# Performance work log

Hardware: AMD Instinct MI355X
Metric: run time of the kernel (lower is better)

The kernel has to match this reference:

```python
import jax, jax.numpy as jnp
import numpy as np

MAX_DELAY = 16
BUF_D = MAX_DELAY + 1  # buffer_max_delay
B, S, I, H, C = 32, 256, 128, 512, 64
OUT_LEN = 64


def setup_inputs() -> dict:
    key = jax.random.key(0)
    ks = jax.random.split(key, 12)
    s = 0.02
    return {
        "x": jax.random.normal(ks[0], (B, S, I), jnp.float32),
        "lengths": jax.random.randint(ks[1], (B,), 0, S, jnp.int32),
        "out_lengths": OUT_LEN,
        "W_in": jax.random.normal(ks[2], (I + H, H), jnp.float32) * s,
        "b_in": jnp.zeros((H,), jnp.float32),
        "W_pass": jax.random.normal(ks[3], (H, H), jnp.float32) * s,
        "b_pass": jnp.zeros((H,), jnp.float32),
        "W_tau": jax.random.normal(ks[4], (H, H), jnp.float32) * s,
        "b_tau": jnp.zeros((H,), jnp.float32),
        "W_mem": jax.random.normal(ks[5], (H, H), jnp.float32) * s,
        "b_mem": jnp.zeros((H,), jnp.float32),
        "W_out": jax.random.normal(ks[6], (H, C), jnp.float32) * s,
        "b_out": jnp.zeros((C,), jnp.float32),
    }


def _update_buffer(buffer, hidden, tau, mem_l):
    # buffer: (B,H,BUF_D); hidden,tau,mem_l: (B,H)
    idx = jnp.arange(1, BUF_D, dtype=buffer.dtype)          # (BUF_D-1,)
    dist = jnp.abs(tau[:, :, None] - idx)                    # (B,H,BUF_D-1)
    w = mem_l[:, :, None] / (1.0 + dist)                     # intensity weights in [0,1]
    nb = buffer[:, :, 1:] + w * hidden[:, :, None]           # shift + weighted write
    return jnp.pad(nb, ((0, 0), (0, 0), (0, 1)))             # F.pad (0,1)


def reference(x, lengths, out_lengths, W_in, b_in, W_pass, b_pass,
              W_tau, b_tau, W_mem, b_mem, W_out, b_out):
    batch, seq_len, _ = x.shape
    hidden = W_pass.shape[0]
    masks = (jnp.arange(seq_len) < lengths[:, None]).astype(x.dtype)  # (B,S)
    buffer0 = jnp.zeros((batch, hidden, BUF_D), x.dtype)

    def encode_step(buffer, inp):
        x_t, m = inp                      # (B,I), (B,)
        h0 = buffer[:, :, 0]
        h = jnp.concatenate([h0, x_t], axis=-1) @ W_in + b_in
        p = h @ W_pass + b_pass
        m = m[:, None]
        h = m * p + (1.0 - m) * h
        tau = jnp.clip(MAX_DELAY * jax.nn.sigmoid(h @ W_tau + b_tau), 1.0, float(MAX_DELAY))
        mem_l = jax.nn.sigmoid(h @ W_mem + b_mem)
        return _update_buffer(buffer, h, tau, mem_l), None

    buffer, _ = jax.lax.scan(encode_step,
                             buffer0,
                             (jnp.swapaxes(x, 0, 1), masks.T))

    def decode_step(buffer, _):
        h0 = buffer[:, :, 0]
        out = h0 @ W_out + b_out
        # x_t is zeros, so concat([h0, 0]) @ W_in == h0 @ W_in[:H]
        h = h0 @ W_in[:hidden] + b_in
        h = h @ W_pass + b_pass
        tau = jnp.clip(MAX_DELAY * jax.nn.sigmoid(h @ W_tau + b_tau), 1.0, float(MAX_DELAY))
        mem_l = jax.nn.sigmoid(h @ W_mem + b_mem)
        return _update_buffer(buffer, h, tau, mem_l), out

    _, outs = jax.lax.scan(decode_step, buffer, None, length=out_lengths)
    return jnp.swapaxes(outs, 0, 1)  # (B, out_lengths, C)
```

## Files before the change

### kernel.cpp

```cpp
#include <hip/hip_runtime.h>
#include <hip/hip_bf16.h>


constexpr int kB    = 32;
constexpr int kS    = 256;
constexpr int kI    = 128;
constexpr int kH    = 512;
constexpr int kC    = 64;
constexpr int kOutL = 64;
constexpr int kMaxD = 16;
constexpr int kBufD = 17;
constexpr int kNWG  = 256;
constexpr int kJPW  = 16;
constexpr int kGrp  = 8;
constexpr int kBpG  = kB / kGrp;
constexpr int kWrd  = kBpG * kH;
constexpr int kSteps = kS + kOutL - 1;
constexpr int kKz   = kH + kI;
constexpr int kZPad = 8;
constexpr unsigned kSpinCap = 131072;

typedef __bf16 bf16x8 __attribute__((ext_vector_type(8)));
typedef float  f32x4  __attribute__((ext_vector_type(4)));
typedef unsigned int u32x4 __attribute__((ext_vector_type(4)));

__device__ __forceinline__ f32x4 MFMA(bf16x8 a, bf16x8 b, f32x4 c) {
  return __builtin_amdgcn_mfma_f32_16x16x32_bf16(a, b, c, 0, 0, 0);
}
__device__ __forceinline__ bf16x8 ld8(const __hip_bfloat16* p) {
  return *reinterpret_cast<const bf16x8*>(p);
}
__device__ __forceinline__ bf16x8 ld8_f32(const float* p) {
  float4 a = *(const float4*)p, b = *(const float4*)(p + 4);
  union { __hip_bfloat16 h[8]; bf16x8 v; } c;
  c.h[0] = __float2bfloat16(a.x); c.h[1] = __float2bfloat16(a.y);
  c.h[2] = __float2bfloat16(a.z); c.h[3] = __float2bfloat16(a.w);
  c.h[4] = __float2bfloat16(b.x); c.h[5] = __float2bfloat16(b.y);
  c.h[6] = __float2bfloat16(b.z); c.h[7] = __float2bfloat16(b.w);
  return c.v;
}
__device__ __forceinline__ float sigm(float x) { return 1.0f / (1.0f + __expf(-x)); }


__global__ void prep_cast(const float* x, const float* W_in, const float* W_pass,
                          const float* W_tau, const float* W_mem, const float* W_out,
                          __hip_bfloat16* xb, __hip_bfloat16* Wall, __hip_bfloat16* BtP,
                          __hip_bfloat16* BtT, __hip_bfloat16* BtM, __hip_bfloat16* WtOut) {
  const int tid = blockIdx.x * blockDim.x + threadIdx.x;
  const int nth = gridDim.x * blockDim.x;
  for (int i = tid; i < kB * kS * kI; i += nth) xb[i] = __float2bfloat16(x[i]);
  for (int i = tid; i < kH * kKz; i += nth) {
    int j = i / kKz, k = i - j * kKz;
    Wall[i] = __float2bfloat16(W_in[k * kH + j]);
  }
  for (int i = tid; i < kH * kH; i += nth) {
    int j = i >> 9, k = i & 511;
    BtP[i] = __float2bfloat16(W_pass[k * kH + j]);
    BtT[i] = __float2bfloat16(W_tau[k * kH + j]);
    BtM[i] = __float2bfloat16(W_mem[k * kH + j]);
  }
  for (int i = tid; i < kC * kH; i += nth) {
    int c = i >> 9, k = i & 511;
    WtOut[i] = __float2bfloat16(W_out[k * kC + c]);
  }
}

__global__ void prep_bias(const float* b_in, const float* b_pass, const float* b_tau,
                          const float* b_mem, const float* W_pass, const float* W_tau,
                          const float* W_mem, float* bias) {
  __shared__ float bp_s[kH];
  const int j = threadIdx.x;
  float s1 = 0.f, s2 = 0.f, s3 = 0.f;
  for (int k = 0; k < kH; ++k) {
    float bi = b_in[k];
    s1 += bi * W_pass[k * kH + j];
    s2 += bi * W_tau[k * kH + j];
    s3 += bi * W_mem[k * kH + j];
  }
  float bP = s1 + b_pass[j];
  bias[j]          = b_in[j];
  bias[kH + j]     = bP;
  bias[2 * kH + j] = s2 + b_tau[j];
  bias[4 * kH + j] = s3 + b_mem[j];
  bp_s[j] = bP;
  __syncthreads();
  float s4 = 0.f, s5 = 0.f;
  for (int k = 0; k < kH; ++k) {
    float v = bp_s[k];
    s4 += v * W_tau[k * kH + j];
    s5 += v * W_mem[k * kH + j];
  }
  bias[3 * kH + j] = s4 + b_tau[j];
  bias[5 * kH + j] = s5 + b_mem[j];
}

__global__ __launch_bounds__(64) void prep_mm1(const float* W_in, const __hip_bfloat16* BtP,
    const __hip_bfloat16* BtT, const __hip_bfloat16* BtM,
    __hip_bfloat16* Wall, __hip_bfloat16* Cip) {
  const int bm = blockIdx.x, bn = blockIdx.y, z = blockIdx.z;
  const int lane = threadIdx.x;
  const int kq = (lane >> 4) * 8;
  const __hip_bfloat16* Bt = (z == 0) ? BtP : (z == 1 ? BtT : BtM);
  const int mat = (z == 0) ? 1 : (z == 1 ? 2 : 4);
  const float* arow = W_in + (size_t)(bm * 16 + (lane & 15)) * kH;
  const __hip_bfloat16* brow = Bt + (size_t)(bn * 16 + (lane & 15)) * kH;
  f32x4 acc = {0.f, 0.f, 0.f, 0.f};
  for (int i = 0; i < 16; ++i) {
    const int kk = i * 32 + kq;
    acc = MFMA(ld8_f32(arow + kk), ld8(brow + kk), acc);
  }
  const int rm = (lane >> 4) * 4, cn = lane & 15;
  union { __hip_bfloat16 h[4]; ushort4 s; } cv;
#pragma unroll
  for (int r = 0; r < 4; ++r) cv.h[r] = __float2bfloat16(acc[r]);
  __hip_bfloat16* wd = Wall + ((size_t)mat * kH + bn * 16 + cn) * kKz + bm * 16 + rm;
  *(ushort4*)wd = cv.s;
  if (z == 0) {
#pragma unroll
    for (int r = 0; r < 4; ++r)
      Cip[(size_t)(bm * 16 + rm + r) * kH + bn * 16 + cn] = cv.h[r];
  }
}

__global__ __launch_bounds__(64) void prep_mm2(const __hip_bfloat16* Cip,
    const __hip_bfloat16* BtT, const __hip_bfloat16* BtM, __hip_bfloat16* Wall) {
  const int bm = blockIdx.x, bn = blockIdx.y, z = blockIdx.z;
  const int lane = threadIdx.x;
  const int kq = (lane >> 4) * 8;
  const __hip_bfloat16* Bt = (z == 0) ? BtT : BtM;
  const int mat = (z == 0) ? 3 : 5;
  const __hip_bfloat16* arow = Cip + (size_t)(bm * 16 + (lane & 15)) * kH;
  const __hip_bfloat16* brow = Bt + (size_t)(bn * 16 + (lane & 15)) * kH;
  f32x4 acc = {0.f, 0.f, 0.f, 0.f};
  for (int i = 0; i < 16; ++i) {
    const int kk = i * 32 + kq;
    acc = MFMA(ld8(arow + kk), ld8(brow + kk), acc);
  }
  const int rm = (lane >> 4) * 4, cn = lane & 15;
  union { __hip_bfloat16 h[4]; ushort4 s; } cv;
#pragma unroll
  for (int r = 0; r < 4; ++r) cv.h[r] = __float2bfloat16(acc[r]);
  __hip_bfloat16* wd = Wall + ((size_t)mat * kH + bn * 16 + cn) * kKz + bm * 16 + rm;
  *(ushort4*)wd = cv.s;
}


struct KParams {
  const __hip_bfloat16* xb;
  const __hip_bfloat16* Wall;
  const __hip_bfloat16* WtOut;
  const float* bias;
  const float* b_out;
  unsigned* h0a;
  unsigned* h0b;
  __hip_bfloat16* h0hist;
  int* arrive;
  const int* lengths;
  float* dout;
};

__global__ __launch_bounds__(256, 1) void rnn_main(KParams P) {
  __shared__ __align__(16) __hip_bfloat16 zs[16][kKz + kZPad];
  __shared__ __align__(16) float outLDS[6][4][16][4];
  __shared__ int len_s[kBpG];

  const int tid = threadIdx.x;
  const int lane = tid & 63, wave = tid >> 6;
  const int kq = (lane >> 4) * 8;
  const int g    = blockIdx.x & 7;
  const int slot = blockIdx.x >> 3;
  const int jn   = slot * kJPW + (lane & 15);
  const int bg0  = kBpG * g;

  bf16x8 wreg[6][5];
#pragma unroll
  for (int m = 0; m < 6; ++m)
#pragma unroll
    for (int i = 0; i < 5; ++i)
      wreg[m][i] = ld8(P.Wall + ((size_t)m * kH + jn) * kKz + wave * 160 + i * 32 + kq);

  if (tid < kBpG) len_s[tid] = P.lengths[bg0 + tid];

  for (int idx = tid; idx < 12 * (kKz + kZPad) / 2; idx += 256)
    ((unsigned*)&zs[4][0])[idx] = 0u;

  if (tid < 64) {
    const int b = tid >> 4, seg = tid & 15;
    *(u32x4*)&zs[b][kH + seg * 8] =
        *(const u32x4*)(P.xb + ((size_t)(bg0 + b) * kS + 0) * kI + seg * 8);
  }

  float bufr[2][kBufD];
#pragma unroll
  for (int u = 0; u < 2; ++u)
#pragma unroll
    for (int d = 0; d < kBufD; ++d) bufr[u][d] = 0.f;

  const int eb = tid >> 3, epr = tid & 7;
  const unsigned o0 = (unsigned)tid * 16u;
  const unsigned o1 = o0 + 4096u;
  unsigned* const h0a_g = P.h0a + (size_t)g * kWrd;
  unsigned* const h0b_g = P.h0b + (size_t)g * kWrd;

  bool dead = false;

  for (int t = 0; t < kSteps; ++t) {
    const unsigned* h0r = (t & 1) ? h0b_g : h0a_g;
    unsigned*       h0w = (t & 1) ? h0a_g : h0b_g;
    const unsigned tga = ((unsigned)t) << 16;
    u32x4 c0, c1;

    for (unsigned spin = 0;; ++spin) {
      asm volatile(
          "global_load_dwordx4 %0, %2, %4 sc1\n\t"
          "global_load_dwordx4 %1, %3, %4 sc1\n\t"
          "s_waitcnt vmcnt(0)"
          : "=&v"(c0), "=&v"(c1)
          : "v"(o0), "v"(o1), "s"(h0r)
          : "memory");
      const unsigned bad = (c0.x ^ tga) | (c0.y ^ tga) | (c0.z ^ tga) | (c0.w ^ tga) |
                           (c1.x ^ tga) | (c1.y ^ tga) | (c1.z ^ tga) | (c1.w ^ tga);
      if ((bad & 0xffff0000u) == 0) break;
      if (dead || spin > kSpinCap) { dead = true; break; }
      __builtin_amdgcn_s_sleep(1);
    }
    {
      const int bb = tid >> 7, c4 = (tid & 127) * 4;
      *(uint2*)&zs[bb][c4] =
          make_uint2((c0.x & 0xffffu) | (c0.y << 16), (c0.z & 0xffffu) | (c0.w << 16));
      *(uint2*)&zs[2 + bb][c4] =
          make_uint2((c1.x & 0xffffu) | (c1.y << 16), (c1.z & 0xffffu) | (c1.w << 16));
    }
    __syncthreads();

    f32x4 a0 = {0.f,0.f,0.f,0.f}, a1 = {0.f,0.f,0.f,0.f}, a2 = {0.f,0.f,0.f,0.f};
    f32x4 a3 = {0.f,0.f,0.f,0.f}, a4 = {0.f,0.f,0.f,0.f}, a5 = {0.f,0.f,0.f,0.f};
    {
      const int ar = lane & 15;
      const int kb = wave * 160 + kq;
#pragma unroll
      for (int i = 0; i < 5; ++i) {
        const bf16x8 av = *(const bf16x8*)&zs[ar][kb + i * 32];
        a0 = MFMA(av, wreg[0][i], a0);
        a1 = MFMA(av, wreg[1][i], a1);
        a2 = MFMA(av, wreg[2][i], a2);
        a3 = MFMA(av, wreg[3][i], a3);
        a4 = MFMA(av, wreg[4][i], a4);
        a5 = MFMA(av, wreg[5][i], a5);
      }
    }
    if (lane < 16) {
      *(f32x4*)&outLDS[0][wave][lane][0] = a0;
      *(f32x4*)&outLDS[1][wave][lane][0] = a1;
      *(f32x4*)&outLDS[2][wave][lane][0] = a2;
      *(f32x4*)&outLDS[3][wave][lane][0] = a3;
      *(f32x4*)&outLDS[4][wave][lane][0] = a4;
      *(f32x4*)&outLDS[5][wave][lane][0] = a5;
    }
    __syncthreads();

    if (tid < 32) {
      const bool msk = (t >= kS) || (t < len_s[eb]);
      float hv2[2], tau2[2], ml2[2];
      unsigned short bits[2];
#pragma unroll
      for (int u = 0; u < 2; ++u) {
        const int cl = epr * 2 + u, j = slot * kJPW + cl;
        float s0 = outLDS[0][0][cl][eb] + outLDS[0][1][cl][eb] + outLDS[0][2][cl][eb] + outLDS[0][3][cl][eb];
        float s1 = outLDS[1][0][cl][eb] + outLDS[1][1][cl][eb] + outLDS[1][2][cl][eb] + outLDS[1][3][cl][eb];
        float s2 = outLDS[2][0][cl][eb] + outLDS[2][1][cl][eb] + outLDS[2][2][cl][eb] + outLDS[2][3][cl][eb];
        float s3 = outLDS[3][0][cl][eb] + outLDS[3][1][cl][eb] + outLDS[3][2][cl][eb] + outLDS[3][3][cl][eb];
        float s4 = outLDS[4][0][cl][eb] + outLDS[4][1][cl][eb] + outLDS[4][2][cl][eb] + outLDS[4][3][cl][eb];
        float s5 = outLDS[5][0][cl][eb] + outLDS[5][1][cl][eb] + outLDS[5][2][cl][eb] + outLDS[5][3][cl][eb];
        const float hp = s0 + P.bias[j];
        const float pv = s1 + P.bias[kH + j];
        const float ta = s2 + P.bias[2 * kH + j];
        const float tb = s3 + P.bias[3 * kH + j];
        const float ma = s4 + P.bias[4 * kH + j];
        const float mb = s5 + P.bias[5 * kH + j];
        const float hv = msk ? pv : hp;
        const float gt = msk ? tb : ta;
        const float gm = msk ? mb : ma;
        float tau = 16.f * sigm(gt);
        tau = fminf(fmaxf(tau, 1.f), 16.f);
        const float ml = sigm(gm);
        hv2[u] = hv; tau2[u] = tau; ml2[u] = ml;
        const float front = bufr[u][1] + (ml / (1.f + fabsf(tau - 1.f))) * hv;
        const __hip_bfloat16 hb = __float2bfloat16(front);
        unsigned short bt;
        __builtin_memcpy(&bt, &hb, 2);
        bits[u] = bt;
      }
      const unsigned tagp = ((unsigned)(t + 1)) << 16;
      const unsigned long long pk =
          ((unsigned long long)(tagp | bits[1]) << 32) | (tagp | bits[0]);
      const unsigned po = (unsigned)((eb * kH + slot * kJPW + epr * 2) * 4);
      asm volatile("global_store_dwordx2 %0, %1, %2 sc1"
                   :: "v"(po), "v"(pk), "s"(h0w) : "memory");

#pragma unroll
      for (int u = 0; u < 2; ++u) {
#pragma unroll
        for (int d = 1; d <= kMaxD; ++d) {
          const float w = ml2[u] / (1.f + fabsf(tau2[u] - (float)d));
          bufr[u][d - 1] = bufr[u][d] + w * hv2[u];
        }
        bufr[u][kMaxD] = 0.f;
      }
      if ((unsigned)(t - (kS - 1)) < (unsigned)kOutL) {
        const unsigned hv = ((unsigned)bits[1] << 16) | bits[0];
        unsigned* hp2 =
            (unsigned*)(P.h0hist + ((size_t)(t - (kS - 1)) * kB + (bg0 + eb)) * kH) +
            (slot * 8 + epr);
        __hip_atomic_store(hp2, hv, __ATOMIC_RELAXED, __HIP_MEMORY_SCOPE_AGENT);
      }
    } else if (wave == 1) {
      const int tn = t + 1;
      const int b = (tid >> 4) & 3, seg = tid & 15;
      if (tn < kS) {
        *(u32x4*)&zs[b][kH + seg * 8] =
            *(const u32x4*)(P.xb + ((size_t)(bg0 + b) * kS + tn) * kI + seg * 8);
      } else if (tn == kS) {
        const u32x4 zv = {0u, 0u, 0u, 0u};
        *(u32x4*)&zs[b][kH + seg * 8] = zv;
      }
    }
  }

  __builtin_amdgcn_s_waitcnt(0);
  __syncthreads();
  const int wg = blockIdx.x;
  if (tid == 0)
    __hip_atomic_store(&P.arrive[wg * 2], 1, __ATOMIC_RELAXED, __HIP_MEMORY_SCOPE_AGENT);
  if (tid < kNWG) {
    unsigned spin = 0;
    while (__hip_atomic_load(&P.arrive[tid * 2],
                             __ATOMIC_RELAXED, __HIP_MEMORY_SCOPE_AGENT) < 1) {
      if (++spin > kSpinCap * 16u) break;
      __builtin_amdgcn_s_sleep(2);
    }
  }
  __syncthreads();
  if (wg >= 32) return;

  {
    const int q = lane >> 4, r = lane & 15;
    const int mrow = wg * 64 + wave * 16 + r;
    const char* ap = (const char*)P.h0hist + (size_t)mrow * 1024 + q * 16;
    u32x4 d0, d1, d2, d3, d4, d5, d6, d7, d8, d9, dA, dB, dC, dD, dE, dF;
    asm volatile(
        "global_load_dwordx4 %0, %16, off sc0 sc1\n\t"
        "global_load_dwordx4 %1, %16, off offset:64 sc0 sc1\n\t"
        "global_load_dwordx4 %2, %16, off offset:128 sc0 sc1\n\t"
        "global_load_dwordx4 %3, %16, off offset:192 sc0 sc1\n\t"
        "global_load_dwordx4 %4, %16, off offset:256 sc0 sc1\n\t"
        "global_load_dwordx4 %5, %16, off offset:320 sc0 sc1\n\t"
        "global_load_dwordx4 %6, %16, off offset:384 sc0 sc1\n\t"
        "global_load_dwordx4 %7, %16, off offset:448 sc0 sc1\n\t"
        "global_load_dwordx4 %8, %16, off offset:512 sc0 sc1\n\t"
        "global_load_dwordx4 %9, %16, off offset:576 sc0 sc1\n\t"
        "global_load_dwordx4 %10, %16, off offset:640 sc0 sc1\n\t"
        "global_load_dwordx4 %11, %16, off offset:704 sc0 sc1\n\t"
        "global_load_dwordx4 %12, %16, off offset:768 sc0 sc1\n\t"
        "global_load_dwordx4 %13, %16, off offset:832 sc0 sc1\n\t"
        "global_load_dwordx4 %14, %16, off offset:896 sc0 sc1\n\t"
        "global_load_dwordx4 %15, %16, off offset:960 sc0 sc1\n\t"
        "s_waitcnt vmcnt(0)"
        : "=&v"(d0), "=&v"(d1), "=&v"(d2), "=&v"(d3),
          "=&v"(d4), "=&v"(d5), "=&v"(d6), "=&v"(d7),
          "=&v"(d8), "=&v"(d9), "=&v"(dA), "=&v"(dB),
          "=&v"(dC), "=&v"(dD), "=&v"(dE), "=&v"(dF)
        : "v"(ap)
        : "memory");
    union { u32x4 u; bf16x8 v; } av[16] = {{d0},{d1},{d2},{d3},{d4},{d5},{d6},{d7},
                                           {d8},{d9},{dA},{dB},{dC},{dD},{dE},{dF}};
    f32x4 T0 = {0.f,0.f,0.f,0.f}, T1 = {0.f,0.f,0.f,0.f};
    f32x4 T2 = {0.f,0.f,0.f,0.f}, T3 = {0.f,0.f,0.f,0.f};
#pragma unroll
    for (int ik = 0; ik < 16; ++ik) {
      const int kk = ik * 32 + kq;
      const __hip_bfloat16* wb = P.WtOut + (size_t)r * kH + kk;
      T0 = MFMA(av[ik].v, ld8(wb), T0);
      T1 = MFMA(av[ik].v, ld8(wb + 16 * kH), T1);
      T2 = MFMA(av[ik].v, ld8(wb + 32 * kH), T2);
      T3 = MFMA(av[ik].v, ld8(wb + 48 * kH), T3);
    }
    f32x4 T[4] = {T0, T1, T2, T3};
#pragma unroll
    for (int ct = 0; ct < 4; ++ct) {
      const int c = ct * 16 + r;
      const float bo = P.b_out[c];
#pragma unroll
      for (int rr = 0; rr < 4; ++rr) {
        const int m = wg * 64 + wave * 16 + q * 4 + rr;
        const int b = m & 31, td = m >> 5;
        P.dout[(size_t)b * (kOutL * kC) + td * kC + c] = T[ct][rr] + bo;
      }
    }
  }
}

extern "C" void kernel_launch(void* const* d_in, const int* in_sizes, int n_in,
                              void* d_out, int out_size, void* d_ws, size_t ws_size,
                              hipStream_t stream) {
  const float* x      = (const float*)d_in[0];
  const int*   lens   = (const int*)d_in[1];
  const float* W_in   = (const float*)d_in[3];
  const float* b_in   = (const float*)d_in[4];
  const float* W_pass = (const float*)d_in[5];
  const float* b_pass = (const float*)d_in[6];
  const float* W_tau  = (const float*)d_in[7];
  const float* b_tau  = (const float*)d_in[8];
  const float* W_mem  = (const float*)d_in[9];
  const float* b_mem  = (const float*)d_in[10];
  const float* W_out  = (const float*)d_in[11];
  const float* b_out  = (const float*)d_in[12];

  char* ws = (char*)d_ws;
  size_t off = 0;
  int* arrive = (int*)(ws + off);                  off += 2048;
  unsigned* h0a = (unsigned*)(ws + off);           off += (size_t)kGrp * kWrd * 4;
  unsigned* h0b = (unsigned*)(ws + off);           off += (size_t)kGrp * kWrd * 4;
  float* bias = (float*)(ws + off);                off += 6 * kH * sizeof(float);
  __hip_bfloat16* WtOut = (__hip_bfloat16*)(ws + off); off += (size_t)kC * kH * 2;
  __hip_bfloat16* h0hist = (__hip_bfloat16*)(ws + off); off += (size_t)kOutL * kB * kH * 2;
  __hip_bfloat16* xb    = (__hip_bfloat16*)(ws + off); off += (size_t)kB * kS * kI * 2;
  __hip_bfloat16* Wall  = (__hip_bfloat16*)(ws + off); off += (size_t)6 * kH * kKz * 2;
  __hip_bfloat16* BtP   = (__hip_bfloat16*)(ws + off); off += (size_t)kH * kH * 2;
  __hip_bfloat16* BtT   = (__hip_bfloat16*)(ws + off); off += (size_t)kH * kH * 2;
  __hip_bfloat16* BtM   = (__hip_bfloat16*)(ws + off); off += (size_t)kH * kH * 2;
  __hip_bfloat16* Cip   = (__hip_bfloat16*)(ws + off); off += (size_t)kKz * kH * 2;

  hipMemsetAsync(d_ws, 0, 2048 + 2 * (size_t)kGrp * kWrd * 4, stream);

  prep_cast<<<512, 256, 0, stream>>>(x, W_in, W_pass, W_tau, W_mem, W_out,
                                     xb, Wall, BtP, BtT, BtM, WtOut);
  prep_bias<<<1, 512, 0, stream>>>(b_in, b_pass, b_tau, b_mem, W_pass, W_tau, W_mem, bias);
  prep_mm1<<<dim3(40, 32, 3), 64, 0, stream>>>(W_in, BtP, BtT, BtM, Wall, Cip);
  prep_mm2<<<dim3(40, 32, 2), 64, 0, stream>>>(Cip, BtT, BtM, Wall);

  KParams P;
  P.xb = xb; P.Wall = Wall; P.WtOut = WtOut; P.bias = bias; P.b_out = b_out;
  P.h0a = h0a; P.h0b = h0b; P.h0hist = h0hist; P.arrive = arrive;
  P.lengths = lens; P.dout = (float*)d_out;

  rnn_main<<<dim3(kNWG), dim3(256), 0, stream>>>(P);
}
```

Measured before the change: 1.093 ms.

## Remove per-step barrier by giving each wave its own K slice and double-buffering x

The K split across waves is remapped so each wave polls, unpacks and consumes only its own 128-wide slice of h0, plus a separate 32-wide slice of x. That lets the first __syncthreads in each step become a per-wave lgkmcnt wait. The x input and the MFMA partial-sum buffers are double-buffered by step parity, so each wave loads the next step's x into registers early and writes it after the MFMA. The h0 exchange layout in global memory is permuted so a wave's slice is contiguous, and the spin loop drops s_sleep and uses a wave-wide any vote. The intent is to cut per-step synchronisation latency in this latency-bound recurrence, at the cost of busier polling and subtler cross-wave ordering.

```diff
diff --git a/kernel.cpp b/kernel.cpp
--- a/kernel.cpp
+++ b/kernel.cpp
@@ -17,7 +17,6 @@
 constexpr int kWrd  = kBpG * kH;
 constexpr int kSteps = kS + kOutL - 1;
 constexpr int kKz   = kH + kI;
-constexpr int kZPad = 8;
 constexpr unsigned kSpinCap = 131072;
 
 typedef __bf16 bf16x8 __attribute__((ext_vector_type(8)));
@@ -160,8 +159,9 @@
 };
 
 __global__ __launch_bounds__(256, 1) void rnn_main(KParams P) {
-  __shared__ __align__(16) __hip_bfloat16 zs[16][kKz + kZPad];
-  __shared__ __align__(16) float outLDS[6][4][16][4];
+  __shared__ __align__(16) __hip_bfloat16 zs[16][520];
+  __shared__ __align__(16) __hip_bfloat16 xs[2][16][136];
+  __shared__ __align__(16) float outLDS[2][6][4][16][4];
   __shared__ int len_s[kBpG];
 
   const int tid = threadIdx.x;
@@ -174,20 +174,19 @@
 
   bf16x8 wreg[6][5];
 #pragma unroll
-  for (int m = 0; m < 6; ++m)
-#pragma unroll
-    for (int i = 0; i < 5; ++i)
-      wreg[m][i] = ld8(P.Wall + ((size_t)m * kH + jn) * kKz + wave * 160 + i * 32 + kq);
+  for (int m = 0; m < 6; ++m) {
+#pragma unroll
+    for (int i = 0; i < 4; ++i)
+      wreg[m][i] = ld8(P.Wall + ((size_t)m * kH + jn) * kKz + wave * 128 + i * 32 + kq);
+    wreg[m][4] = ld8(P.Wall + ((size_t)m * kH + jn) * kKz + 512 + wave * 32 + kq);
+  }
 
   if (tid < kBpG) len_s[tid] = P.lengths[bg0 + tid];
 
-  for (int idx = tid; idx < 12 * (kKz + kZPad) / 2; idx += 256)
-    ((unsigned*)&zs[4][0])[idx] = 0u;
-
-  if (tid < 64) {
-    const int b = tid >> 4, seg = tid & 15;
-    *(u32x4*)&zs[b][kH + seg * 8] =
-        *(const u32x4*)(P.xb + ((size_t)(bg0 + b) * kS + 0) * kI + seg * 8);
+  {
+    const int b = lane >> 4, c2 = (lane & 15) * 2;
+    *(unsigned*)&xs[0][b][wave * 32 + c2] =
+        *(const unsigned*)(P.xb + ((size_t)(bg0 + b) * kS + 0) * kI + wave * 32 + c2);
   }
 
   float bufr[2][kBufD];
@@ -197,8 +196,7 @@
     for (int d = 0; d < kBufD; ++d) bufr[u][d] = 0.f;
 
   const int eb = tid >> 3, epr = tid & 7;
-  const unsigned o0 = (unsigned)tid * 16u;
-  const unsigned o1 = o0 + 4096u;
+  const unsigned ow = (unsigned)((wave * 512 + lane * 8) * 4);
   unsigned* const h0a_g = P.h0a + (size_t)g * kWrd;
   unsigned* const h0b_g = P.h0b + (size_t)g * kWrd;
 
@@ -212,35 +210,48 @@
 
     for (unsigned spin = 0;; ++spin) {
       asm volatile(
-          "global_load_dwordx4 %0, %2, %4 sc1\n\t"
-          "global_load_dwordx4 %1, %3, %4 sc1\n\t"
+          "global_load_dwordx4 %0, %2, %3 sc1\n\t"
+          "global_load_dwordx4 %1, %2, %3 offset:16 sc1\n\t"
           "s_waitcnt vmcnt(0)"
           : "=&v"(c0), "=&v"(c1)
-          : "v"(o0), "v"(o1), "s"(h0r)
+          : "v"(ow), "s"(h0r)
           : "memory");
       const unsigned bad = (c0.x ^ tga) | (c0.y ^ tga) | (c0.z ^ tga) | (c0.w ^ tga) |
                            (c1.x ^ tga) | (c1.y ^ tga) | (c1.z ^ tga) | (c1.w ^ tga);
-      if ((bad & 0xffff0000u) == 0) break;
+      if (!__any((int)((bad & 0xffff0000u) != 0))) break;
       if (dead || spin > kSpinCap) { dead = true; break; }
-      __builtin_amdgcn_s_sleep(1);
-    }
+    }
+
+    const int tn = t + 1;
+    const int xbr = lane >> 4, xc2 = (lane & 15) * 2;
+    unsigned xreg = 0;
+    bool xst = false;
+    if (tn < kS) {
+      xreg = *(const unsigned*)(P.xb + ((size_t)(bg0 + xbr) * kS + tn) * kI + wave * 32 + xc2);
+      xst = true;
+    } else if (tn <= kS + 1) {
+      xst = true;
+    }
+
     {
-      const int bb = tid >> 7, c4 = (tid & 127) * 4;
-      *(uint2*)&zs[bb][c4] =
-          make_uint2((c0.x & 0xffffu) | (c0.y << 16), (c0.z & 0xffffu) | (c0.w << 16));
-      *(uint2*)&zs[2 + bb][c4] =
-          make_uint2((c1.x & 0xffffu) | (c1.y << 16), (c1.z & 0xffffu) | (c1.w << 16));
-    }
-    __syncthreads();
+      const int b = lane >> 4;
+      u32x4 p;
+      p.x = (c0.x & 0xffffu) | (c0.y << 16);
+      p.y = (c0.z & 0xffffu) | (c0.w << 16);
+      p.z = (c1.x & 0xffffu) | (c1.y << 16);
+      p.w = (c1.z & 0xffffu) | (c1.w << 16);
+      *(u32x4*)&zs[b][wave * 128 + (lane & 15) * 8] = p;
+    }
+    asm volatile("s_waitcnt lgkmcnt(0)" ::: "memory");
+    __builtin_amdgcn_sched_barrier(0);
 
     f32x4 a0 = {0.f,0.f,0.f,0.f}, a1 = {0.f,0.f,0.f,0.f}, a2 = {0.f,0.f,0.f,0.f};
     f32x4 a3 = {0.f,0.f,0.f,0.f}, a4 = {0.f,0.f,0.f,0.f}, a5 = {0.f,0.f,0.f,0.f};
     {
       const int ar = lane & 15;
-      const int kb = wave * 160 + kq;
-#pragma unroll
-      for (int i = 0; i < 5; ++i) {
-        const bf16x8 av = *(const bf16x8*)&zs[ar][kb + i * 32];
+#pragma unroll
+      for (int i = 0; i < 4; ++i) {
+        const bf16x8 av = *(const bf16x8*)&zs[ar][wave * 128 + i * 32 + kq];
         a0 = MFMA(av, wreg[0][i], a0);
         a1 = MFMA(av, wreg[1][i], a1);
         a2 = MFMA(av, wreg[2][i], a2);
@@ -248,30 +259,40 @@
         a4 = MFMA(av, wreg[4][i], a4);
         a5 = MFMA(av, wreg[5][i], a5);
       }
+      const bf16x8 av = *(const bf16x8*)&xs[t & 1][ar][wave * 32 + kq];
+      a0 = MFMA(av, wreg[0][4], a0);
+      a1 = MFMA(av, wreg[1][4], a1);
+      a2 = MFMA(av, wreg[2][4], a2);
+      a3 = MFMA(av, wreg[3][4], a3);
+      a4 = MFMA(av, wreg[4][4], a4);
+      a5 = MFMA(av, wreg[5][4], a5);
     }
     if (lane < 16) {
-      *(f32x4*)&outLDS[0][wave][lane][0] = a0;
-      *(f32x4*)&outLDS[1][wave][lane][0] = a1;
-      *(f32x4*)&outLDS[2][wave][lane][0] = a2;
-      *(f32x4*)&outLDS[3][wave][lane][0] = a3;
-      *(f32x4*)&outLDS[4][wave][lane][0] = a4;
-      *(f32x4*)&outLDS[5][wave][lane][0] = a5;
-    }
+      *(f32x4*)&outLDS[t & 1][0][wave][lane][0] = a0;
+      *(f32x4*)&outLDS[t & 1][1][wave][lane][0] = a1;
+      *(f32x4*)&outLDS[t & 1][2][wave][lane][0] = a2;
+      *(f32x4*)&outLDS[t & 1][3][wave][lane][0] = a3;
+      *(f32x4*)&outLDS[t & 1][4][wave][lane][0] = a4;
+      *(f32x4*)&outLDS[t & 1][5][wave][lane][0] = a5;
+    }
+    if (xst) *(unsigned*)&xs[tn & 1][xbr][wave * 32 + xc2] = xreg;
+
     __syncthreads();
 
     if (tid < 32) {
+      const int op = t & 1;
       const bool msk = (t >= kS) || (t < len_s[eb]);
       float hv2[2], tau2[2], ml2[2];
       unsigned short bits[2];
 #pragma unroll
       for (int u = 0; u < 2; ++u) {
         const int cl = epr * 2 + u, j = slot * kJPW + cl;
-        float s0 = outLDS[0][0][cl][eb] + outLDS[0][1][cl][eb] + outLDS[0][2][cl][eb] + outLDS[0][3][cl][eb];
-        float s1 = outLDS[1][0][cl][eb] + outLDS[1][1][cl][eb] + outLDS[1][2][cl][eb] + outLDS[1][3][cl][eb];
-        float s2 = outLDS[2][0][cl][eb] + outLDS[2][1][cl][eb] + outLDS[2][2][cl][eb] + outLDS[2][3][cl][eb];
-        float s3 = outLDS[3][0][cl][eb] + outLDS[3][1][cl][eb] + outLDS[3][2][cl][eb] + outLDS[3][3][cl][eb];
-        float s4 = outLDS[4][0][cl][eb] + outLDS[4][1][cl][eb] + outLDS[4][2][cl][eb] + outLDS[4][3][cl][eb];
-        float s5 = outLDS[5][0][cl][eb] + outLDS[5][1][cl][eb] + outLDS[5][2][cl][eb] + outLDS[5][3][cl][eb];
+        float s0 = outLDS[op][0][0][cl][eb] + outLDS[op][0][1][cl][eb] + outLDS[op][0][2][cl][eb] + outLDS[op][0][3][cl][eb];
+        float s1 = outLDS[op][1][0][cl][eb] + outLDS[op][1][1][cl][eb] + outLDS[op][1][2][cl][eb] + outLDS[op][1][3][cl][eb];
+        float s2 = outLDS[op][2][0][cl][eb] + outLDS[op][2][1][cl][eb] + outLDS[op][2][2][cl][eb] + outLDS[op][2][3][cl][eb];
+        float s3 = outLDS[op][3][0][cl][eb] + outLDS[op][3][1][cl][eb] + outLDS[op][3][2][cl][eb] + outLDS[op][3][3][cl][eb];
+        float s4 = outLDS[op][4][0][cl][eb] + outLDS[op][4][1][cl][eb] + outLDS[op][4][2][cl][eb] + outLDS[op][4][3][cl][eb];
+        float s5 = outLDS[op][5][0][cl][eb] + outLDS[op][5][1][cl][eb] + outLDS[op][5][2][cl][eb] + outLDS[op][5][3][cl][eb];
         const float hp = s0 + P.bias[j];
         const float pv = s1 + P.bias[kH + j];
         const float ta = s2 + P.bias[2 * kH + j];
@@ -294,7 +315,8 @@
       const unsigned tagp = ((unsigned)(t + 1)) << 16;
       const unsigned long long pk =
           ((unsigned long long)(tagp | bits[1]) << 32) | (tagp | bits[0]);
-      const unsigned po = (unsigned)((eb * kH + slot * kJPW + epr * 2) * 4);
+      const unsigned po =
+          (unsigned)((((slot >> 3) * 512) + eb * 128 + (slot & 7) * 16 + epr * 2) * 4);
       asm volatile("global_store_dwordx2 %0, %1, %2 sc1"
                    :: "v"(po), "v"(pk), "s"(h0w) : "memory");
 
@@ -313,16 +335,6 @@
             (unsigned*)(P.h0hist + ((size_t)(t - (kS - 1)) * kB + (bg0 + eb)) * kH) +
             (slot * 8 + epr);
         __hip_atomic_store(hp2, hv, __ATOMIC_RELAXED, __HIP_MEMORY_SCOPE_AGENT);
-      }
-    } else if (wave == 1) {
-      const int tn = t + 1;
-      const int b = (tid >> 4) & 3, seg = tid & 15;
-      if (tn < kS) {
-        *(u32x4*)&zs[b][kH + seg * 8] =
-            *(const u32x4*)(P.xb + ((size_t)(bg0 + b) * kS + tn) * kI + seg * 8);
-      } else if (tn == kS) {
-        const u32x4 zv = {0u, 0u, 0u, 0u};
-        *(u32x4*)&zs[b][kH + seg * 8] = zv;
       }
     }
   }
```

Measured after the change: 1.105 ms. Within noise of the previous version (+1.1%).
